# Optimization experiments

Hardware: AMD Instinct MI355X
Metric: run time of the kernel (lower is better)

The kernel has to match this reference:

```python
import jax, jax.numpy as jnp
import numpy as np
from jax import lax

W_SCALE = 0.1   # brevitas SignedBinaryWeightPerTensorConst default scaling_init
A_SCALE = 1.0   # SignedBinaryActPerTensorConst: min/max = -1/1 -> scale 1
BN_EPS = 1e-5


def _bin_w(w):
    # sign(w) * const scale, straight-through estimator (identity STE as in brevitas binary_sign_ste)
    q = jnp.where(w >= 0, W_SCALE, -W_SCALE).astype(w.dtype)
    return w + lax.stop_gradient(q - w)


def _bin_act(x):
    # QuantHardTanh with binary act quant: output is sign(x)*1, STE passes grad inside [-1,1]
    c = jnp.clip(x, -A_SCALE, A_SCALE)
    q = jnp.where(x >= 0, A_SCALE, -A_SCALE).astype(x.dtype)
    return c + lax.stop_gradient(q - c)


def _conv(x, w, b, stride=(1, 1), pad=((0, 0), (0, 0))):
    y = lax.conv_general_dilated(x, _bin_w(w), window_strides=stride, padding=pad,
                                 dimension_numbers=('NCHW', 'OIHW', 'NCHW'))
    return y + b[None, :, None, None]


def _bn(x, gamma, beta):
    # training-mode BatchNorm2d: batch statistics over (N, H, W)
    mu = jnp.mean(x, axis=(0, 2, 3), keepdims=True)
    var = jnp.var(x, axis=(0, 2, 3), keepdims=True)
    inv = lax.rsqrt(var + BN_EPS)
    return (x - mu) * inv * gamma[None, :, None, None] + beta[None, :, None, None]


def _pool2x1(x):
    # MaxPool2d((2,1)) with floor: drop trailing odd row
    N, C, H, W = x.shape
    h2 = H // 2
    return x[:, :, : 2 * h2].reshape(N, C, h2, 2, W).max(axis=3)


def setup_inputs() -> dict:
    key = jax.random.key(0)
    ks = jax.random.split(key, 10)
    nC = 128
    d = {
        'x':  jax.random.normal(ks[0], (64, 1, 16000, 1), jnp.float32),
        'w1': jax.random.normal(ks[1], (nC, 1, 84, 1), jnp.float32) * 0.05,
        'b1': jnp.zeros((nC,), jnp.float32),
        'g1': jnp.ones((nC,), jnp.float32), 'be1': jnp.zeros((nC,), jnp.float32),
        'w2': jax.random.normal(ks[2], (nC, nC, 4, 1), jnp.float32) * 0.05,
        'b2': jnp.zeros((nC,), jnp.float32),
        'g2': jnp.ones((nC,), jnp.float32), 'be2': jnp.zeros((nC,), jnp.float32),
        'w3': jax.random.normal(ks[3], (2 * nC, nC, 4, 1), jnp.float32) * 0.05,
        'b3': jnp.zeros((2 * nC,), jnp.float32),
        'g3': jnp.ones((2 * nC,), jnp.float32), 'be3': jnp.zeros((2 * nC,), jnp.float32),
        'w5': jax.random.normal(ks[4], (4 * nC, 2 * nC, 3, 1), jnp.float32) * 0.05,
        'b5': jnp.zeros((4 * nC,), jnp.float32),
        'g5': jnp.ones((4 * nC,), jnp.float32), 'be5': jnp.zeros((4 * nC,), jnp.float32),
        'wfc': jax.random.normal(ks[5], (35, 4 * nC * 249), jnp.float32) * 0.01,
    }
    return d


def reference(x, w1, b1, g1, be1, w2, b2, g2, be2, w3, b3, g3, be3,
              w5, b5, g5, be5, wfc):
    h = _conv(x, w1, b1, stride=(4, 1))                     # [B,128,3980,1]
    h = _pool2x1(_bin_act(_bn(h, g1, be1)))                 # [B,128,1990,1]
    h = _conv(h, w2, b2, pad=((2, 2), (0, 0)))              # [B,128,1991,1]
    h = _pool2x1(_bin_act(_bn(h, g2, be2)))                 # [B,128,995,1]
    h = _conv(h, w3, b3, pad=((1, 1), (0, 0)))              # [B,256,994,1]
    h = _pool2x1(_bin_act(_bn(h, g3, be3)))                 # [B,256,497,1]
    h = _conv(h, w5, b5, pad=((2, 2), (0, 0)))              # [B,512,499,1]
    h = _pool2x1(_bin_act(_bn(h, g5, be5)))                 # [B,512,249,1]
    h = h.reshape(h.shape[0], -1)                           # [B, 512*249]
    return h @ _bin_w(wfc).T                                # [B, 35]
```

## Files before the change

### kernel.cpp

```cpp
#include <hip/hip_runtime.h>
#include <stdint.h>


constexpr int Bn  = 64;
constexpr int H1  = 3980;
constexpr int J1  = 1990;
constexpr int H2o = 1991, J2 = 995;
constexpr int H3o = 994,  J3 = 497;
constexpr int H5o = 499,  J5 = 249;
constexpr int FCW = 249 * 8;
constexpr int NSH = 16;
constexpr int QS2 = 0;
constexpr int QS3 = 4096;
constexpr int QS5 = 12288;
constexpr int QS_TOTAL = 28672;

__global__ __launch_bounds__(256) void prep_all(
    const float* __restrict__ w2, const float* __restrict__ w3,
    const float* __restrict__ w5, const float* __restrict__ wfc,
    const float* __restrict__ w1,
    uint64_t* __restrict__ wb2, uint64_t* __restrict__ wb3,
    uint64_t* __restrict__ wb5, uint64_t* __restrict__ wbf,
    float* __restrict__ w1pk, unsigned long long* __restrict__ qs)
{
    const int bx  = blockIdx.x;
    const int idx = bx * 256 + threadIdx.x;
    if (idx < QS_TOTAL) qs[idx] = 0ull;

    if (bx < 78) {
        if (idx < 1024) {
            int wdx = idx & 1, k = (idx >> 1) & 3, c = idx >> 3;
            uint64_t v = 0;
            for (int ci = 0; ci < 64; ++ci)
                if (w2[((size_t)c * 128 + (wdx * 64 + ci)) * 4 + k] >= 0.f) v |= 1ull << ci;
            wb2[idx] = v;
        } else if (idx < 3072) {
            int t = idx - 1024;
            int wdx = t & 1, k = (t >> 1) & 3, c = t >> 3;
            uint64_t v = 0;
            for (int ci = 0; ci < 64; ++ci)
                if (w3[((size_t)c * 128 + (wdx * 64 + ci)) * 4 + k] >= 0.f) v |= 1ull << ci;
            wb3[t] = v;
        } else if (idx < 9216) {
            int t = idx - 3072;
            int wdx = t & 3, k = (t >> 2) % 3, c = t / 12;
            uint64_t v = 0;
            for (int ci = 0; ci < 64; ++ci)
                if (w5[((size_t)c * 256 + (wdx * 64 + ci)) * 3 + k] >= 0.f) v |= 1ull << ci;
            wb5[t] = v;
        } else if (idx < 9216 + 10752) {
            int t  = idx - 9216;
            int G  = t / 672, r = t % 672;
            int kg = r >> 5;
            int e  = r & 31;
            int u  = e >> 2, jj = e & 3;
            w1pk[t] = (w1[(size_t)(G * 8 + u) * 84 + kg * 4 + jj] >= 0.f) ? 0.1f : -0.1f;
        }
    } else {
        const int t = bx - 78;
        const int oc = t >> 3, wdx = t & 7;
        const int wave = threadIdx.x >> 6, lane = threadIdx.x & 63;
        const int hh = wave * 64 + lane;
        const bool ok = hh < 249;
        const float* src = wfc + (size_t)oc * 127488 + (size_t)wdx * 64 * 249 + hh;
        uint64_t word = 0;
        #pragma unroll 8
        for (int c = 0; c < 64; ++c) {
            const float v = ok ? src[(size_t)c * 249] : -1.f;
            if (v >= 0.f) word |= 1ull << c;
        }
        if (ok) wbf[(size_t)oc * FCW + (size_t)hh * 8 + wdx] = word;
    }
}

#define ROW_FMA(A, XV) \
    A[u] = fmaf(wv.x, XV.x, A[u]); A[u] = fmaf(wv.y, XV.y, A[u]); \
    A[u] = fmaf(wv.z, XV.z, A[u]); A[u] = fmaf(wv.w, XV.w, A[u]);
#define ROW_STAT(A, HOFF) { \
    const int h = h0 + (HOFF) + tid; \
    if (h < H1) { const float v = A[u] + bv; base[h] = v; \
                  s += (double)v; q += (double)v * v; } }

__global__ __launch_bounds__(256) void conv1_y1(
    const float* __restrict__ x, const float4* __restrict__ w1pk,
    const float* __restrict__ b1, float* __restrict__ y1,
    double2* __restrict__ part)
{
    __shared__ float4 xs4[2068];
    __shared__ float4 wl[336];
    __shared__ double2 statw[4][16];
    const int n   = blockIdx.y;
    const int bh  = blockIdx.x;
    const int h0  = bh << 11;
    const int z   = blockIdx.z;
    const int tid = threadIdx.x;
    const int wave = tid >> 6, lane = tid & 63;

    const float4* x4 = (const float4*)x + (size_t)n * 4000;
    for (int i = tid; i < 2068; i += 256) {
        const int gi = h0 + i;
        xs4[i] = (gi < 4000) ? x4[gi] : make_float4(0.f, 0.f, 0.f, 0.f);
    }
    const float4* wsrc = w1pk + (size_t)z * 336;
    for (int i = tid; i < 336; i += 256) wl[i] = wsrc[i];
    __syncthreads();

    for (int g = 0; g < 2; ++g) {
        float a0[8] = {0,0,0,0,0,0,0,0};
        float a1r[8] = {0,0,0,0,0,0,0,0};
        float a2[8] = {0,0,0,0,0,0,0,0};
        float a3[8] = {0,0,0,0,0,0,0,0};
        float a4[8] = {0,0,0,0,0,0,0,0};
        float a5[8] = {0,0,0,0,0,0,0,0};
        float a6[8] = {0,0,0,0,0,0,0,0};
        float a7[8] = {0,0,0,0,0,0,0,0};
        #pragma unroll 3
        for (int kg = 0; kg < 21; ++kg) {
            const float4 xv0 = xs4[tid + kg];
            const float4 xv1 = xs4[tid + 256 + kg];
            const float4 xv2 = xs4[tid + 512 + kg];
            const float4 xv3 = xs4[tid + 768 + kg];
            const float4 xv4 = xs4[tid + 1024 + kg];
            const float4 xv5 = xs4[tid + 1280 + kg];
            const float4 xv6 = xs4[tid + 1536 + kg];
            const float4 xv7 = xs4[tid + 1792 + kg];
            const float4* wk = &wl[(g * 21 + kg) * 8];
            #pragma unroll
            for (int u = 0; u < 8; ++u) {
                const float4 wv = wk[u];
                ROW_FMA(a0, xv0)
                ROW_FMA(a1r, xv1)
                ROW_FMA(a2, xv2)
                ROW_FMA(a3, xv3)
                ROW_FMA(a4, xv4)
                ROW_FMA(a5, xv5)
                ROW_FMA(a6, xv6)
                ROW_FMA(a7, xv7)
            }
        }
        #pragma unroll
        for (int u = 0; u < 8; ++u) {
            const int c = z * 16 + g * 8 + u;
            const float bv = b1[c];
            float* base = y1 + ((size_t)n * 128 + c) * H1;
            double s = 0.0, q = 0.0;
            ROW_STAT(a0, 0)
            ROW_STAT(a1r, 256)
            ROW_STAT(a2, 512)
            ROW_STAT(a3, 768)
            ROW_STAT(a4, 1024)
            ROW_STAT(a5, 1280)
            ROW_STAT(a6, 1536)
            ROW_STAT(a7, 1792)
            #pragma unroll
            for (int o = 32; o > 0; o >>= 1) {
                s += __shfl_xor(s, o, 64);
                q += __shfl_xor(q, o, 64);
            }
            if (lane == 0) statw[wave][g * 8 + u] = make_double2(s, q);
        }
    }
    __syncthreads();
    if (tid < 16) {
        const double2 p0 = statw[0][tid], p1v = statw[1][tid];
        const double2 p2 = statw[2][tid], p3  = statw[3][tid];
        part[((size_t)((n * 2 + bh) * 8 + z)) * 16 + tid] =
            make_double2(((p0.x + p1v.x) + p2.x) + p3.x,
                         ((p0.y + p1v.y) + p2.y) + p3.y);
    }
}

__global__ __launch_bounds__(128) void bn_reduce1(const double2* __restrict__ part,
                                                  float2* __restrict__ bnp)
{
    __shared__ double sS[128], sQ[128];
    const int c = blockIdx.x, t = threadIdx.x;
    const int z = c >> 4, cl = c & 15;
    const double2 p = part[((size_t)(t * 8 + z)) * 16 + cl];
    sS[t] = p.x; sQ[t] = p.y;
    __syncthreads();
    for (int o = 64; o > 0; o >>= 1) {
        if (t < o) { sS[t] += sS[t + o]; sQ[t] += sQ[t + o]; }
        __syncthreads();
    }
    if (t == 0) {
        const double N = (double)Bn * H1;
        const double mu  = sS[0] / N;
        const double var = sQ[0] / N - mu * mu;
        bnp[c] = make_float2((float)mu, (float)(1.0 / sqrt(var + 1e-5)));
    }
}

__global__ __launch_bounds__(256) void signpool1_y(
    const float* __restrict__ y1, const float2* __restrict__ bnp,
    const float* __restrict__ g1, const float* __restrict__ be1,
    uint32_t* __restrict__ a1_32)
{
    __shared__ float2 smi[128];
    __shared__ float  sg[128], sbe[128];
    const int n    = blockIdx.y;
    const int half = blockIdx.z;
    const int tid  = threadIdx.x;
    if (tid < 128) { smi[tid] = bnp[tid]; sg[tid] = g1[tid]; sbe[tid] = be1[tid]; }
    __syncthreads();
    const int j2  = blockIdx.x * 128 + (tid & 127);
    const int sub = tid >> 7;
    if (j2 >= 995) return;
    const int cbase = half * 64 + sub * 32;
    uint32_t wa = 0, wb = 0;
    for (int i = 0; i < 32; ++i) {
        const int c = cbase + i;
        const float4 v = *(const float4*)(y1 + ((size_t)n * 128 + c) * H1 + 4 * j2);
        const float2 mi = smi[c];
        const float gg = sg[c], bb = sbe[c];
        const float t0 = __fadd_rn(__fmul_rn(__fmul_rn(__fsub_rn(v.x, mi.x), mi.y), gg), bb);
        const float t1 = __fadd_rn(__fmul_rn(__fmul_rn(__fsub_rn(v.y, mi.x), mi.y), gg), bb);
        const float t2 = __fadd_rn(__fmul_rn(__fmul_rn(__fsub_rn(v.z, mi.x), mi.y), gg), bb);
        const float t3 = __fadd_rn(__fmul_rn(__fmul_rn(__fsub_rn(v.w, mi.x), mi.y), gg), bb);
        if ((t0 >= 0.f) || (t1 >= 0.f)) wa |= 1u << i;
        if ((t2 >= 0.f) || (t3 >= 0.f)) wb |= 1u << i;
    }
    const size_t w0 = ((size_t)n * J1 + 2 * j2) * 2 + half;
    a1_32[w0 * 2 + sub]       = wa;
    a1_32[(w0 + 2) * 2 + sub] = wb;
}

template<int CINW, int KK, int PAD, int COUT>
__global__ __launch_bounds__(COUT) void bconv_stats(
    const uint64_t* __restrict__ ain, const uint64_t* __restrict__ wb,
    const int HIN, const int HOUT, unsigned long long* __restrict__ qs)
{
    constexpr int RW = 64 + KK - 1;
    __shared__ ulonglong2 rows2[RW * CINW / 2];
    uint64_t* rows = (uint64_t*)rows2;
    const int n  = blockIdx.y;
    const int h0 = blockIdx.x << 6;
    const int c  = threadIdx.x;
    for (int i = c; i < RW * CINW; i += COUT) {
        int r = h0 - PAD + i / CINW;
        rows[i] = (r >= 0 && r < HIN) ? ain[((size_t)n * HIN + r) * CINW + (i % CINW)] : 0ull;
    }
    __syncthreads();
    uint64_t wreg[KK * CINW];
    #pragma unroll
    for (int i = 0; i < KK * CINW; ++i) wreg[i] = wb[(size_t)c * KK * CINW + i];
    int pcw[KK];
    #pragma unroll
    for (int k = 0; k < KK; ++k) {
        int pc = 0;
        #pragma unroll
        for (int wd = 0; wd < CINW; ++wd) pc += __popcll(wreg[k * CINW + wd]);
        pcw[k] = pc;
    }
    int sq = 0, sq2 = 0;
    const int hmax = min(64, HOUT - h0);
    int i = 0;
    for (; i + 1 < hmax; i += 2) {
        uint64_t win[(KK + 1) * CINW];
        #pragma unroll
        for (int t = 0; t < (KK + 1) * CINW / 2; ++t) {
            const ulonglong2 v = rows2[i * (CINW / 2) + t];
            win[2 * t] = v.x; win[2 * t + 1] = v.y;
        }
        int X0 = 0, X1 = 0;
        #pragma unroll
        for (int k = 0; k < KK; ++k)
            #pragma unroll
            for (int wd = 0; wd < CINW; ++wd) {
                X0 += __popcll(win[k * CINW + wd] ^ wreg[k * CINW + wd]);
                X1 += __popcll(win[(k + 1) * CINW + wd] ^ wreg[k * CINW + wd]);
            }
        int q0 = 64 * CINW * KK - 2 * X0;
        int q1 = 64 * CINW * KK - 2 * X1;
        const int h = h0 + i;
        if (h < PAD || h + 1 > HIN + PAD - KK) {
            #pragma unroll
            for (int k = 0; k < KK; ++k) {
                if (k < PAD - h || k >= HIN + PAD - h)
                    q0 -= 64 * CINW - 2 * pcw[k];
                if (k < PAD - (h + 1) || k >= HIN + PAD - (h + 1))
                    q1 -= 64 * CINW - 2 * pcw[k];
            }
        }
        sq += q0 + q1; sq2 += q0 * q0 + q1 * q1;
    }
    if (i < hmax) {
        const int h = h0 + i;
        int X = 0;
        #pragma unroll
        for (int k = 0; k < KK; ++k)
            #pragma unroll
            for (int wd = 0; wd < CINW; ++wd)
                X += __popcll(rows[(i + k) * CINW + wd] ^ wreg[k * CINW + wd]);
        int q = 64 * CINW * KK - 2 * X;
        if (h < PAD || h > HIN + PAD - KK) {
            #pragma unroll
            for (int k = 0; k < KK; ++k)
                if (k < PAD - h || k >= HIN + PAD - h)
                    q -= 64 * CINW - 2 * pcw[k];
        }
        sq += q; sq2 += q * q;
    }
    const int sh = (blockIdx.x + blockIdx.y) & (NSH - 1);
    atomicAdd(&qs[((size_t)sh * COUT + c) * 2 + 0], (unsigned long long)(long long)sq);
    atomicAdd(&qs[((size_t)sh * COUT + c) * 2 + 1], (unsigned long long)(long long)sq2);
}

template<int CINW, int KK, int PAD, int COUT>
__global__ __launch_bounds__(COUT) void bconv_sign(
    const uint64_t* __restrict__ ain, const uint64_t* __restrict__ wb,
    const int HIN, const int HOUT, const int J, const double N,
    const float* __restrict__ bias, const unsigned long long* __restrict__ qs,
    const float* __restrict__ g, const float* __restrict__ be,
    uint64_t* __restrict__ aout)
{
    constexpr int W = COUT / 64;
    constexpr int RW = 64 + KK - 1;
    __shared__ ulonglong2 rows2[RW * CINW / 2];
    uint64_t* rows = (uint64_t*)rows2;
    const int n  = blockIdx.y;
    const int h0 = blockIdx.x << 6;
    const int c  = threadIdx.x;
    for (int i = c; i < RW * CINW; i += COUT) {
        int r = h0 - PAD + i / CINW;
        rows[i] = (r >= 0 && r < HIN) ? ain[((size_t)n * HIN + r) * CINW + (i % CINW)] : 0ull;
    }
    long long Sq = 0, Sq2 = 0;
    #pragma unroll
    for (int s = 0; s < NSH; ++s) {
        Sq  += (long long)qs[((size_t)s * COUT + c) * 2 + 0];
        Sq2 += (long long)qs[((size_t)s * COUT + c) * 2 + 1];
    }
    const double bb_d = (double)bias[c];
    const double S  = 0.1 * (double)Sq + N * bb_d;
    const double SS = 0.01 * (double)Sq2 + 0.2 * bb_d * (double)Sq + N * bb_d * bb_d;
    const double mu = S / N;
    const double var = SS / N - mu * mu;
    const float2 mi = make_float2((float)mu, (float)(1.0 / sqrt(var + 1e-5)));
    __syncthreads();
    uint64_t wreg[KK * CINW];
    #pragma unroll
    for (int i = 0; i < KK * CINW; ++i) wreg[i] = wb[(size_t)c * KK * CINW + i];
    int pcw[KK];
    #pragma unroll
    for (int k = 0; k < KK; ++k) {
        int pc = 0;
        #pragma unroll
        for (int wd = 0; wd < CINW; ++wd) pc += __popcll(wreg[k * CINW + wd]);
        pcw[k] = pc;
    }
    const float bb = bias[c], gg = g[c], bbe = be[c];
    const int wv = c >> 6, lane = c & 63;
    const int hmax = min(64, HOUT - h0);
    for (int i = 0; i + 1 < hmax; i += 2) {
        uint64_t win[(KK + 1) * CINW];
        #pragma unroll
        for (int t = 0; t < (KK + 1) * CINW / 2; ++t) {
            const ulonglong2 v = rows2[i * (CINW / 2) + t];
            win[2 * t] = v.x; win[2 * t + 1] = v.y;
        }
        int X0 = 0, X1 = 0;
        #pragma unroll
        for (int k = 0; k < KK; ++k)
            #pragma unroll
            for (int wd = 0; wd < CINW; ++wd) {
                X0 += __popcll(win[k * CINW + wd] ^ wreg[k * CINW + wd]);
                X1 += __popcll(win[(k + 1) * CINW + wd] ^ wreg[k * CINW + wd]);
            }
        int q0 = 64 * CINW * KK - 2 * X0;
        int q1 = 64 * CINW * KK - 2 * X1;
        const int h = h0 + i;
        if (h < PAD || h + 1 > HIN + PAD - KK) {
            #pragma unroll
            for (int k = 0; k < KK; ++k) {
                if (k < PAD - h || k >= HIN + PAD - h)
                    q0 -= 64 * CINW - 2 * pcw[k];
                if (k < PAD - (h + 1) || k >= HIN + PAD - (h + 1))
                    q1 -= 64 * CINW - 2 * pcw[k];
            }
        }
        const float y0 = __fadd_rn(__fmul_rn(0.1f, (float)q0), bb);
        const float y1v = __fadd_rn(__fmul_rn(0.1f, (float)q1), bb);
        const float t0 = __fadd_rn(__fmul_rn(__fmul_rn(__fsub_rn(y0,  mi.x), mi.y), gg), bbe);
        const float t1 = __fadd_rn(__fmul_rn(__fmul_rn(__fsub_rn(y1v, mi.x), mi.y), gg), bbe);
        const uint64_t word = __ballot(t0 >= 0.f) | __ballot(t1 >= 0.f);
        const int j = h >> 1;
        if (lane == 0 && j < J)
            aout[((size_t)n * J + j) * W + wv] = word;
    }
}

__global__ void fc_kernel(const uint64_t* __restrict__ a5, const uint64_t* __restrict__ wfcb,
                          float* __restrict__ out)
{
    const int n    = blockIdx.y;
    const int oc   = blockIdx.x * 4 + (threadIdx.x >> 6);
    const int lane = threadIdx.x & 63;
    if (oc >= 35) return;
    const uint64_t* arow = a5   + (size_t)n  * FCW;
    const uint64_t* wrow = wfcb + (size_t)oc * FCW;
    int X = 0;
    for (int i = lane; i < FCW; i += 64)
        X += __popcll(arow[i] ^ wrow[i]);
    for (int o = 32; o > 0; o >>= 1) X += __shfl_xor(X, o, 64);
    if (lane == 0) out[(size_t)n * 35 + oc] = 0.1f * (float)(127488 - 2 * X);
}

extern "C" void kernel_launch(void* const* d_in, const int* in_sizes, int n_in,
                              void* d_out, int out_size, void* d_ws, size_t ws_size,
                              hipStream_t stream)
{
    (void)in_sizes; (void)n_in; (void)out_size;
    const float* x   = (const float*)d_in[0];
    const float* w1  = (const float*)d_in[1];
    const float* b1  = (const float*)d_in[2];
    const float* g1  = (const float*)d_in[3];
    const float* be1 = (const float*)d_in[4];
    const float* w2  = (const float*)d_in[5];
    const float* b2  = (const float*)d_in[6];
    const float* g2  = (const float*)d_in[7];
    const float* be2 = (const float*)d_in[8];
    const float* w3  = (const float*)d_in[9];
    const float* b3  = (const float*)d_in[10];
    const float* g3  = (const float*)d_in[11];
    const float* be3 = (const float*)d_in[12];
    const float* w5  = (const float*)d_in[13];
    const float* b5  = (const float*)d_in[14];
    const float* g5  = (const float*)d_in[15];
    const float* be5 = (const float*)d_in[16];
    const float* wfc = (const float*)d_in[17];
    char* ws = (char*)d_ws;

    size_t cur = 0;
    auto take = [&](size_t bytes) {
        size_t r = cur;
        cur = (cur + bytes + 255) & ~(size_t)255;
        return r;
    };
    const size_t off_y1 = take(130416640);
    float*    y1  = (float*)(ws + off_y1);
    uint64_t* a1  = (uint64_t*)(ws + take(2037760));
    uint64_t* a2  = (uint64_t*)(ws + take(1018880));
    uint64_t* a3  = (uint64_t*)(ws + take(1017856));
    uint64_t* a5  = (uint64_t*)(ws + take(1019904));
    uint64_t* wb2 = (uint64_t*)(ws + take(8192));
    uint64_t* wb3 = (uint64_t*)(ws + take(16384));
    uint64_t* wb5 = (uint64_t*)(ws + take(49152));
    uint64_t* wbf = (uint64_t*)(ws + take(557760));
    float*    w1pk = (float*)(ws + take(43008));
    double2*  p1  = (double2*)(ws + take(262144));
    unsigned long long* qs = (unsigned long long*)(ws + take(QS_TOTAL * 8));
    float2*   bnp1 = (float2*)(ws + take(1024));
    if (cur > ws_size) return;

    hipLaunchKernelGGL(prep_all, dim3(358), dim3(256), 0, stream,
                       w2, w3, w5, wfc, w1, wb2, wb3, wb5, wbf, w1pk, qs);
    hipLaunchKernelGGL(conv1_y1, dim3(2, 64, 8), dim3(256), 0, stream,
                       x, (const float4*)w1pk, b1, y1, p1);
    hipLaunchKernelGGL(bn_reduce1, dim3(128), dim3(128), 0, stream, p1, bnp1);
    hipLaunchKernelGGL(signpool1_y, dim3(8, 64, 2), dim3(256), 0, stream,
                       y1, bnp1, g1, be1, (uint32_t*)a1);
    hipLaunchKernelGGL((bconv_stats<2, 4, 2, 128>), dim3(32, 64), dim3(128), 0, stream,
                       a1, wb2, J1, H2o, qs + QS2);
    hipLaunchKernelGGL((bconv_sign<2, 4, 2, 128>), dim3(32, 64), dim3(128), 0, stream,
                       a1, wb2, J1, H2o, J2, (double)Bn * H2o, b2, qs + QS2, g2, be2, a2);
    hipLaunchKernelGGL((bconv_stats<2, 4, 1, 256>), dim3(16, 64), dim3(256), 0, stream,
                       a2, wb3, J2, H3o, qs + QS3);
    hipLaunchKernelGGL((bconv_sign<2, 4, 1, 256>), dim3(16, 64), dim3(256), 0, stream,
                       a2, wb3, J2, H3o, J3, (double)Bn * H3o, b3, qs + QS3, g3, be3, a3);
    hipLaunchKernelGGL((bconv_stats<4, 3, 2, 512>), dim3(8, 64), dim3(512), 0, stream,
                       a3, wb5, J3, H5o, qs + QS5);
    hipLaunchKernelGGL((bconv_sign<4, 3, 2, 512>), dim3(8, 64), dim3(512), 0, stream,
                       a3, wb5, J3, H5o, J5, (double)Bn * H5o, b5, qs + QS5, g5, be5, a5);
    hipLaunchKernelGGL(fc_kernel, dim3(9, 64), dim3(256), 0, stream,
                       a5, wbf, (float*)d_out);
}
```

Before: 304.2 us.

## Fuse post-conv1 stages into one cooperative persistent kernel with grid syncs

Replaces the chain of small kernels (BN reduce, sign-pool, three conv stats/sign pairs, FC) with a single cooperative kernel of 512 persistent blocks. Grid-wide syncs separate the phases, and blocks loop over virtual blocks. Conv phases now use fixed 256-thread blocks and split rows or channels to fit that size. The goal is to remove per-kernel launch and drain overhead between many short stages. The cost is the grid.sync barriers, fewer resident blocks per phase, and register pressure from one large kernel.

After: 726.9 us. +139.0%, slower.

```diff
diff --git a/kernel.cpp b/kernel.cpp
--- a/kernel.cpp
+++ b/kernel.cpp
@@ -1,5 +1,8 @@
 #include <hip/hip_runtime.h>
+#include <hip/hip_cooperative_groups.h>
 #include <stdint.h>
+
+namespace cg = cooperative_groups;
 
 
 constexpr int Bn  = 64;
@@ -14,6 +17,7 @@
 constexpr int QS3 = 4096;
 constexpr int QS5 = 12288;
 constexpr int QS_TOTAL = 28672;
+constexpr int MEGA_BLOCKS = 512;
 
 __global__ __launch_bounds__(256) void prep_all(
     const float* __restrict__ w2, const float* __restrict__ w3,
@@ -170,240 +174,244 @@
     }
 }
 
-__global__ __launch_bounds__(128) void bn_reduce1(const double2* __restrict__ part,
-                                                  float2* __restrict__ bnp)
+struct MegaArgs {
+    const double2* p1;
+    float2* bnp1;
+    const float* g1; const float* be1;
+    const float* y1;
+    uint32_t* a1_32;
+    const uint64_t* a1;
+    const uint64_t* wb2; const uint64_t* wb3; const uint64_t* wb5;
+    const uint64_t* wbf;
+    unsigned long long* qs;
+    const float* b2; const float* g2; const float* be2;
+    const float* b3; const float* g3; const float* be3;
+    const float* b5; const float* g5; const float* be5;
+    uint64_t* a2; uint64_t* a3; uint64_t* a5;
+    float* out;
+};
+
+template<int CINW, int KK, int PAD, int COUT, int NSUB, int CSPL, bool SIGN>
+__device__ void bconv_phase(const uint64_t* __restrict__ ain,
+                            const uint64_t* __restrict__ wbt,
+                            const int HIN, const int HOUT, const int J,
+                            const double N, const float* __restrict__ bias,
+                            unsigned long long* __restrict__ qs,
+                            const float* __restrict__ g, const float* __restrict__ be,
+                            uint64_t* __restrict__ aout, ulonglong2* rows2)
 {
+    constexpr int CPB = COUT / CSPL;
+    constexpr int TR  = 64 * NSUB;
+    constexpr int WR  = TR + KK - 1;
+    constexpr int W   = COUT / 64;
+    uint64_t* rows = (uint64_t*)rows2;
+    const int tid = threadIdx.x;
+    const int sub = tid / CPB;
+    const int cl  = tid % CPB;
+    const int ntiles = (HOUT + TR - 1) / TR;
+    const int nvb = ntiles * CSPL * 64;
+
+    for (int vb = blockIdx.x; vb < nvb; vb += gridDim.x) {
+        const int tile  = vb % ntiles;
+        const int rest  = vb / ntiles;
+        const int chunk = rest % CSPL;
+        const int n     = rest / CSPL;
+        const int c     = chunk * CPB + cl;
+        const int h0    = tile * TR;
+        __syncthreads();
+        for (int i = tid; i < WR * CINW; i += 256) {
+            const int r = h0 - PAD + i / CINW;
+            rows[i] = (r >= 0 && r < HIN) ? ain[((size_t)n * HIN + r) * CINW + (i % CINW)] : 0ull;
+        }
+        __syncthreads();
+        uint64_t wreg[KK * CINW];
+        #pragma unroll
+        for (int i2 = 0; i2 < KK * CINW; ++i2) wreg[i2] = wbt[(size_t)c * KK * CINW + i2];
+        int pcw[KK];
+        #pragma unroll
+        for (int k = 0; k < KK; ++k) {
+            int pc = 0;
+            #pragma unroll
+            for (int wd = 0; wd < CINW; ++wd) pc += __popcll(wreg[k * CINW + wd]);
+            pcw[k] = pc;
+        }
+        const int hb   = h0 + sub * 64;
+        const int hmax = min(64, HOUT - hb);
+        float2 mi = make_float2(0.f, 0.f);
+        float bb = 0.f, gg = 0.f, bbe = 0.f;
+        if constexpr (SIGN) {
+            long long Sq = 0, Sq2 = 0;
+            #pragma unroll
+            for (int s = 0; s < NSH; ++s) {
+                Sq  += (long long)qs[((size_t)s * COUT + c) * 2 + 0];
+                Sq2 += (long long)qs[((size_t)s * COUT + c) * 2 + 1];
+            }
+            const double bb_d = (double)bias[c];
+            const double S  = 0.1 * (double)Sq + N * bb_d;
+            const double SS = 0.01 * (double)Sq2 + 0.2 * bb_d * (double)Sq + N * bb_d * bb_d;
+            const double mu = S / N;
+            const double var = SS / N - mu * mu;
+            mi = make_float2((float)mu, (float)(1.0 / sqrt(var + 1e-5)));
+            bb = bias[c]; gg = g[c]; bbe = be[c];
+        }
+        int sq = 0, sq2 = 0;
+        int i = 0;
+        for (; i + 1 < hmax; i += 2) {
+            const int l = sub * 64 + i;
+            uint64_t win[(KK + 1) * CINW];
+            #pragma unroll
+            for (int t2 = 0; t2 < (KK + 1) * CINW / 2; ++t2) {
+                const ulonglong2 v = rows2[l * (CINW / 2) + t2];
+                win[2 * t2] = v.x; win[2 * t2 + 1] = v.y;
+            }
+            int X0 = 0, X1 = 0;
+            #pragma unroll
+            for (int k = 0; k < KK; ++k)
+                #pragma unroll
+                for (int wd = 0; wd < CINW; ++wd) {
+                    X0 += __popcll(win[k * CINW + wd] ^ wreg[k * CINW + wd]);
+                    X1 += __popcll(win[(k + 1) * CINW + wd] ^ wreg[k * CINW + wd]);
+                }
+            int q0 = 64 * CINW * KK - 2 * X0;
+            int q1 = 64 * CINW * KK - 2 * X1;
+            const int h = hb + i;
+            if (h < PAD || h + 1 > HIN + PAD - KK) {
+                #pragma unroll
+                for (int k = 0; k < KK; ++k) {
+                    if (k < PAD - h || k >= HIN + PAD - h)
+                        q0 -= 64 * CINW - 2 * pcw[k];
+                    if (k < PAD - (h + 1) || k >= HIN + PAD - (h + 1))
+                        q1 -= 64 * CINW - 2 * pcw[k];
+                }
+            }
+            if constexpr (SIGN) {
+                const float y0  = __fadd_rn(__fmul_rn(0.1f, (float)q0), bb);
+                const float y1v = __fadd_rn(__fmul_rn(0.1f, (float)q1), bb);
+                const float t0 = __fadd_rn(__fmul_rn(__fmul_rn(__fsub_rn(y0,  mi.x), mi.y), gg), bbe);
+                const float t1 = __fadd_rn(__fmul_rn(__fmul_rn(__fsub_rn(y1v, mi.x), mi.y), gg), bbe);
+                const uint64_t word = __ballot(t0 >= 0.f) | __ballot(t1 >= 0.f);
+                const int j = h >> 1;
+                if ((c & 63) == 0 && j < J)
+                    aout[((size_t)n * J + j) * W + (c >> 6)] = word;
+            } else {
+                sq += q0 + q1; sq2 += q0 * q0 + q1 * q1;
+            }
+        }
+        if constexpr (!SIGN) {
+            if (i < hmax) {
+                const int l = sub * 64 + i;
+                const int h = hb + i;
+                int X = 0;
+                #pragma unroll
+                for (int k = 0; k < KK; ++k)
+                    #pragma unroll
+                    for (int wd = 0; wd < CINW; ++wd)
+                        X += __popcll(rows[(l + k) * CINW + wd] ^ wreg[k * CINW + wd]);
+                int q = 64 * CINW * KK - 2 * X;
+                if (h < PAD || h > HIN + PAD - KK) {
+                    #pragma unroll
+                    for (int k = 0; k < KK; ++k)
+                        if (k < PAD - h || k >= HIN + PAD - h)
+                            q -= 64 * CINW - 2 * pcw[k];
+                }
+                sq += q; sq2 += q * q;
+            }
+            const int sh = vb & (NSH - 1);
+            atomicAdd(&qs[((size_t)sh * COUT + c) * 2 + 0], (unsigned long long)(long long)sq);
+            atomicAdd(&qs[((size_t)sh * COUT + c) * 2 + 1], (unsigned long long)(long long)sq2);
+        }
+    }
+}
+
+__global__ __launch_bounds__(256) void mega(MegaArgs A)
+{
+    cg::grid_group grid = cg::this_grid();
     __shared__ double sS[128], sQ[128];
-    const int c = blockIdx.x, t = threadIdx.x;
-    const int z = c >> 4, cl = c & 15;
-    const double2 p = part[((size_t)(t * 8 + z)) * 16 + cl];
-    sS[t] = p.x; sQ[t] = p.y;
+    __shared__ float2 smi[128];
+    __shared__ float  sgm[128], sbe[128];
+    __shared__ ulonglong2 rows2[132];
+    const int tid = threadIdx.x;
+
+    if (blockIdx.x < 128) {
+        const int c = blockIdx.x;
+        const int z = c >> 4, cl = c & 15;
+        if (tid < 128) {
+            const double2 p = A.p1[((size_t)(tid * 8 + z)) * 16 + cl];
+            sS[tid] = p.x; sQ[tid] = p.y;
+        }
+        __syncthreads();
+        for (int o = 64; o > 0; o >>= 1) {
+            if (tid < o) { sS[tid] += sS[tid + o]; sQ[tid] += sQ[tid + o]; }
+            __syncthreads();
+        }
+        if (tid == 0) {
+            const double N = (double)Bn * H1;
+            const double mu  = sS[0] / N;
+            const double var = sQ[0] / N - mu * mu;
+            A.bnp1[c] = make_float2((float)mu, (float)(1.0 / sqrt(var + 1e-5)));
+        }
+    }
+    grid.sync();
+
+    if (tid < 128) { smi[tid] = A.bnp1[tid]; sgm[tid] = A.g1[tid]; sbe[tid] = A.be1[tid]; }
     __syncthreads();
-    for (int o = 64; o > 0; o >>= 1) {
-        if (t < o) { sS[t] += sS[t + o]; sQ[t] += sQ[t + o]; }
-        __syncthreads();
-    }
-    if (t == 0) {
-        const double N = (double)Bn * H1;
-        const double mu  = sS[0] / N;
-        const double var = sQ[0] / N - mu * mu;
-        bnp[c] = make_float2((float)mu, (float)(1.0 / sqrt(var + 1e-5)));
-    }
-}
-
-__global__ __launch_bounds__(256) void signpool1_y(
-    const float* __restrict__ y1, const float2* __restrict__ bnp,
-    const float* __restrict__ g1, const float* __restrict__ be1,
-    uint32_t* __restrict__ a1_32)
-{
-    __shared__ float2 smi[128];
-    __shared__ float  sg[128], sbe[128];
-    const int n    = blockIdx.y;
-    const int half = blockIdx.z;
-    const int tid  = threadIdx.x;
-    if (tid < 128) { smi[tid] = bnp[tid]; sg[tid] = g1[tid]; sbe[tid] = be1[tid]; }
-    __syncthreads();
-    const int j2  = blockIdx.x * 128 + (tid & 127);
-    const int sub = tid >> 7;
-    if (j2 >= 995) return;
-    const int cbase = half * 64 + sub * 32;
-    uint32_t wa = 0, wb = 0;
-    for (int i = 0; i < 32; ++i) {
-        const int c = cbase + i;
-        const float4 v = *(const float4*)(y1 + ((size_t)n * 128 + c) * H1 + 4 * j2);
-        const float2 mi = smi[c];
-        const float gg = sg[c], bb = sbe[c];
-        const float t0 = __fadd_rn(__fmul_rn(__fmul_rn(__fsub_rn(v.x, mi.x), mi.y), gg), bb);
-        const float t1 = __fadd_rn(__fmul_rn(__fmul_rn(__fsub_rn(v.y, mi.x), mi.y), gg), bb);
-        const float t2 = __fadd_rn(__fmul_rn(__fmul_rn(__fsub_rn(v.z, mi.x), mi.y), gg), bb);
-        const float t3 = __fadd_rn(__fmul_rn(__fmul_rn(__fsub_rn(v.w, mi.x), mi.y), gg), bb);
-        if ((t0 >= 0.f) || (t1 >= 0.f)) wa |= 1u << i;
-        if ((t2 >= 0.f) || (t3 >= 0.f)) wb |= 1u << i;
-    }
-    const size_t w0 = ((size_t)n * J1 + 2 * j2) * 2 + half;
-    a1_32[w0 * 2 + sub]       = wa;
-    a1_32[(w0 + 2) * 2 + sub] = wb;
-}
-
-template<int CINW, int KK, int PAD, int COUT>
-__global__ __launch_bounds__(COUT) void bconv_stats(
-    const uint64_t* __restrict__ ain, const uint64_t* __restrict__ wb,
-    const int HIN, const int HOUT, unsigned long long* __restrict__ qs)
-{
-    constexpr int RW = 64 + KK - 1;
-    __shared__ ulonglong2 rows2[RW * CINW / 2];
-    uint64_t* rows = (uint64_t*)rows2;
-    const int n  = blockIdx.y;
-    const int h0 = blockIdx.x << 6;
-    const int c  = threadIdx.x;
-    for (int i = c; i < RW * CINW; i += COUT) {
-        int r = h0 - PAD + i / CINW;
-        rows[i] = (r >= 0 && r < HIN) ? ain[((size_t)n * HIN + r) * CINW + (i % CINW)] : 0ull;
-    }
-    __syncthreads();
-    uint64_t wreg[KK * CINW];
-    #pragma unroll
-    for (int i = 0; i < KK * CINW; ++i) wreg[i] = wb[(size_t)c * KK * CINW + i];
-    int pcw[KK];
-    #pragma unroll
-    for (int k = 0; k < KK; ++k) {
-        int pc = 0;
+    for (int vb = blockIdx.x; vb < 1024; vb += gridDim.x) {
+        const int bx = vb & 7, n = (vb >> 3) & 63, half = vb >> 9;
+        const int j2 = bx * 128 + (tid & 127);
+        const int sub = tid >> 7;
+        if (j2 < 995) {
+            const int cbase = half * 64 + sub * 32;
+            uint32_t wa = 0, wbv = 0;
+            for (int i = 0; i < 32; ++i) {
+                const int c = cbase + i;
+                const float4 v = *(const float4*)(A.y1 + ((size_t)n * 128 + c) * H1 + 4 * j2);
+                const float2 mi = smi[c];
+                const float gg = sgm[c], bb = sbe[c];
+                const float t0 = __fadd_rn(__fmul_rn(__fmul_rn(__fsub_rn(v.x, mi.x), mi.y), gg), bb);
+                const float t1 = __fadd_rn(__fmul_rn(__fmul_rn(__fsub_rn(v.y, mi.x), mi.y), gg), bb);
+                const float t2 = __fadd_rn(__fmul_rn(__fmul_rn(__fsub_rn(v.z, mi.x), mi.y), gg), bb);
+                const float t3 = __fadd_rn(__fmul_rn(__fmul_rn(__fsub_rn(v.w, mi.x), mi.y), gg), bb);
+                if ((t0 >= 0.f) || (t1 >= 0.f)) wa  |= 1u << i;
+                if ((t2 >= 0.f) || (t3 >= 0.f)) wbv |= 1u << i;
+            }
+            const size_t w0 = ((size_t)n * J1 + 2 * j2) * 2 + half;
+            A.a1_32[w0 * 2 + sub]       = wa;
+            A.a1_32[(w0 + 2) * 2 + sub] = wbv;
+        }
+    }
+    grid.sync();
+
+    bconv_phase<2, 4, 2, 128, 2, 1, false>(A.a1, A.wb2, J1, H2o, 0, 0.0, nullptr,
+                                           A.qs + QS2, nullptr, nullptr, nullptr, rows2);
+    grid.sync();
+    bconv_phase<2, 4, 2, 128, 2, 1, true>(A.a1, A.wb2, J1, H2o, J2, (double)Bn * H2o,
+                                          A.b2, A.qs + QS2, A.g2, A.be2, A.a2, rows2);
+    grid.sync();
+    bconv_phase<2, 4, 1, 256, 1, 1, false>(A.a2, A.wb3, J2, H3o, 0, 0.0, nullptr,
+                                           A.qs + QS3, nullptr, nullptr, nullptr, rows2);
+    grid.sync();
+    bconv_phase<2, 4, 1, 256, 1, 1, true>(A.a2, A.wb3, J2, H3o, J3, (double)Bn * H3o,
+                                          A.b3, A.qs + QS3, A.g3, A.be3, A.a3, rows2);
+    grid.sync();
+    bconv_phase<4, 3, 2, 512, 1, 2, false>(A.a3, A.wb5, J3, H5o, 0, 0.0, nullptr,
+                                           A.qs + QS5, nullptr, nullptr, nullptr, rows2);
+    grid.sync();
+    bconv_phase<4, 3, 2, 512, 1, 2, true>(A.a3, A.wb5, J3, H5o, J5, (double)Bn * H5o,
+                                          A.b5, A.qs + QS5, A.g5, A.be5, A.a5, rows2);
+    grid.sync();
+
+    for (int t = blockIdx.x * 4 + (tid >> 6); t < 64 * 35; t += gridDim.x * 4) {
+        const int n = t / 35, oc = t % 35;
+        const int lane = tid & 63;
+        const uint64_t* arow = A.a5  + (size_t)n  * FCW;
+        const uint64_t* wrow = A.wbf + (size_t)oc * FCW;
+        int X = 0;
+        for (int i = lane; i < FCW; i += 64)
+            X += __popcll(arow[i] ^ wrow[i]);
         #pragma unroll
-        for (int wd = 0; wd < CINW; ++wd) pc += __popcll(wreg[k * CINW + wd]);
-        pcw[k] = pc;
-    }
-    int sq = 0, sq2 = 0;
-    const int hmax = min(64, HOUT - h0);
-    int i = 0;
-    for (; i + 1 < hmax; i += 2) {
-        uint64_t win[(KK + 1) * CINW];
-        #pragma unroll
-        for (int t = 0; t < (KK + 1) * CINW / 2; ++t) {
-            const ulonglong2 v = rows2[i * (CINW / 2) + t];
-            win[2 * t] = v.x; win[2 * t + 1] = v.y;
-        }
-        int X0 = 0, X1 = 0;
-        #pragma unroll
-        for (int k = 0; k < KK; ++k)
-            #pragma unroll
-            for (int wd = 0; wd < CINW; ++wd) {
-                X0 += __popcll(win[k * CINW + wd] ^ wreg[k * CINW + wd]);
-                X1 += __popcll(win[(k + 1) * CINW + wd] ^ wreg[k * CINW + wd]);
-            }
-        int q0 = 64 * CINW * KK - 2 * X0;
-        int q1 = 64 * CINW * KK - 2 * X1;
-        const int h = h0 + i;
-        if (h < PAD || h + 1 > HIN + PAD - KK) {
-            #pragma unroll
-            for (int k = 0; k < KK; ++k) {
-                if (k < PAD - h || k >= HIN + PAD - h)
-                    q0 -= 64 * CINW - 2 * pcw[k];
-                if (k < PAD - (h + 1) || k >= HIN + PAD - (h + 1))
-                    q1 -= 64 * CINW - 2 * pcw[k];
-            }
-        }
-        sq += q0 + q1; sq2 += q0 * q0 + q1 * q1;
-    }
-    if (i < hmax) {
-        const int h = h0 + i;
-        int X = 0;
-        #pragma unroll
-        for (int k = 0; k < KK; ++k)
-            #pragma unroll
-            for (int wd = 0; wd < CINW; ++wd)
-                X += __popcll(rows[(i + k) * CINW + wd] ^ wreg[k * CINW + wd]);
-        int q = 64 * CINW * KK - 2 * X;
-        if (h < PAD || h > HIN + PAD - KK) {
-            #pragma unroll
-            for (int k = 0; k < KK; ++k)
-                if (k < PAD - h || k >= HIN + PAD - h)
-                    q -= 64 * CINW - 2 * pcw[k];
-        }
-        sq += q; sq2 += q * q;
-    }
-    const int sh = (blockIdx.x + blockIdx.y) & (NSH - 1);
-    atomicAdd(&qs[((size_t)sh * COUT + c) * 2 + 0], (unsigned long long)(long long)sq);
-    atomicAdd(&qs[((size_t)sh * COUT + c) * 2 + 1], (unsigned long long)(long long)sq2);
-}
-
-template<int CINW, int KK, int PAD, int COUT>
-__global__ __launch_bounds__(COUT) void bconv_sign(
-    const uint64_t* __restrict__ ain, const uint64_t* __restrict__ wb,
-    const int HIN, const int HOUT, const int J, const double N,
-    const float* __restrict__ bias, const unsigned long long* __restrict__ qs,
-    const float* __restrict__ g, const float* __restrict__ be,
-    uint64_t* __restrict__ aout)
-{
-    constexpr int W = COUT / 64;
-    constexpr int RW = 64 + KK - 1;
-    __shared__ ulonglong2 rows2[RW * CINW / 2];
-    uint64_t* rows = (uint64_t*)rows2;
-    const int n  = blockIdx.y;
-    const int h0 = blockIdx.x << 6;
-    const int c  = threadIdx.x;
-    for (int i = c; i < RW * CINW; i += COUT) {
-        int r = h0 - PAD + i / CINW;
-        rows[i] = (r >= 0 && r < HIN) ? ain[((size_t)n * HIN + r) * CINW + (i % CINW)] : 0ull;
-    }
-    long long Sq = 0, Sq2 = 0;
-    #pragma unroll
-    for (int s = 0; s < NSH; ++s) {
-        Sq  += (long long)qs[((size_t)s * COUT + c) * 2 + 0];
-        Sq2 += (long long)qs[((size_t)s * COUT + c) * 2 + 1];
-    }
-    const double bb_d = (double)bias[c];
-    const double S  = 0.1 * (double)Sq + N * bb_d;
-    const double SS = 0.01 * (double)Sq2 + 0.2 * bb_d * (double)Sq + N * bb_d * bb_d;
-    const double mu = S / N;
-    const double var = SS / N - mu * mu;
-    const float2 mi = make_float2((float)mu, (float)(1.0 / sqrt(var + 1e-5)));
-    __syncthreads();
-    uint64_t wreg[KK * CINW];
-    #pragma unroll
-    for (int i = 0; i < KK * CINW; ++i) wreg[i] = wb[(size_t)c * KK * CINW + i];
-    int pcw[KK];
-    #pragma unroll
-    for (int k = 0; k < KK; ++k) {
-        int pc = 0;
-        #pragma unroll
-        for (int wd = 0; wd < CINW; ++wd) pc += __popcll(wreg[k * CINW + wd]);
-        pcw[k] = pc;
-    }
-    const float bb = bias[c], gg = g[c], bbe = be[c];
-    const int wv = c >> 6, lane = c & 63;
-    const int hmax = min(64, HOUT - h0);
-    for (int i = 0; i + 1 < hmax; i += 2) {
-        uint64_t win[(KK + 1) * CINW];
-        #pragma unroll
-        for (int t = 0; t < (KK + 1) * CINW / 2; ++t) {
-            const ulonglong2 v = rows2[i * (CINW / 2) + t];
-            win[2 * t] = v.x; win[2 * t + 1] = v.y;
-        }
-        int X0 = 0, X1 = 0;
-        #pragma unroll
-        for (int k = 0; k < KK; ++k)
-            #pragma unroll
-            for (int wd = 0; wd < CINW; ++wd) {
-                X0 += __popcll(win[k * CINW + wd] ^ wreg[k * CINW + wd]);
-                X1 += __popcll(win[(k + 1) * CINW + wd] ^ wreg[k * CINW + wd]);
-            }
-        int q0 = 64 * CINW * KK - 2 * X0;
-        int q1 = 64 * CINW * KK - 2 * X1;
-        const int h = h0 + i;
-        if (h < PAD || h + 1 > HIN + PAD - KK) {
-            #pragma unroll
-            for (int k = 0; k < KK; ++k) {
-                if (k < PAD - h || k >= HIN + PAD - h)
-                    q0 -= 64 * CINW - 2 * pcw[k];
-                if (k < PAD - (h + 1) || k >= HIN + PAD - (h + 1))
-                    q1 -= 64 * CINW - 2 * pcw[k];
-            }
-        }
-        const float y0 = __fadd_rn(__fmul_rn(0.1f, (float)q0), bb);
-        const float y1v = __fadd_rn(__fmul_rn(0.1f, (float)q1), bb);
-        const float t0 = __fadd_rn(__fmul_rn(__fmul_rn(__fsub_rn(y0,  mi.x), mi.y), gg), bbe);
-        const float t1 = __fadd_rn(__fmul_rn(__fmul_rn(__fsub_rn(y1v, mi.x), mi.y), gg), bbe);
-        const uint64_t word = __ballot(t0 >= 0.f) | __ballot(t1 >= 0.f);
-        const int j = h >> 1;
-        if (lane == 0 && j < J)
-            aout[((size_t)n * J + j) * W + wv] = word;
-    }
-}
-
-__global__ void fc_kernel(const uint64_t* __restrict__ a5, const uint64_t* __restrict__ wfcb,
-                          float* __restrict__ out)
-{
-    const int n    = blockIdx.y;
-    const int oc   = blockIdx.x * 4 + (threadIdx.x >> 6);
-    const int lane = threadIdx.x & 63;
-    if (oc >= 35) return;
-    const uint64_t* arow = a5   + (size_t)n  * FCW;
-    const uint64_t* wrow = wfcb + (size_t)oc * FCW;
-    int X = 0;
-    for (int i = lane; i < FCW; i += 64)
-        X += __popcll(arow[i] ^ wrow[i]);
-    for (int o = 32; o > 0; o >>= 1) X += __shfl_xor(X, o, 64);
-    if (lane == 0) out[(size_t)n * 35 + oc] = 0.1f * (float)(127488 - 2 * X);
+        for (int o = 32; o > 0; o >>= 1) X += __shfl_xor(X, o, 64);
+        if (lane == 0) A.out[(size_t)n * 35 + oc] = 0.1f * (float)(127488 - 2 * X);
+    }
 }
 
 extern "C" void kernel_launch(void* const* d_in, const int* in_sizes, int n_in,
@@ -457,21 +465,18 @@
                        w2, w3, w5, wfc, w1, wb2, wb3, wb5, wbf, w1pk, qs);
     hipLaunchKernelGGL(conv1_y1, dim3(2, 64, 8), dim3(256), 0, stream,
                        x, (const float4*)w1pk, b1, y1, p1);
-    hipLaunchKernelGGL(bn_reduce1, dim3(128), dim3(128), 0, stream, p1, bnp1);
-    hipLaunchKernelGGL(signpool1_y, dim3(8, 64, 2), dim3(256), 0, stream,
-                       y1, bnp1, g1, be1, (uint32_t*)a1);
-    hipLaunchKernelGGL((bconv_stats<2, 4, 2, 128>), dim3(32, 64), dim3(128), 0, stream,
-                       a1, wb2, J1, H2o, qs + QS2);
-    hipLaunchKernelGGL((bconv_sign<2, 4, 2, 128>), dim3(32, 64), dim3(128), 0, stream,
-                       a1, wb2, J1, H2o, J2, (double)Bn * H2o, b2, qs + QS2, g2, be2, a2);
-    hipLaunchKernelGGL((bconv_stats<2, 4, 1, 256>), dim3(16, 64), dim3(256), 0, stream,
-                       a2, wb3, J2, H3o, qs + QS3);
-    hipLaunchKernelGGL((bconv_sign<2, 4, 1, 256>), dim3(16, 64), dim3(256), 0, stream,
-                       a2, wb3, J2, H3o, J3, (double)Bn * H3o, b3, qs + QS3, g3, be3, a3);
-    hipLaunchKernelGGL((bconv_stats<4, 3, 2, 512>), dim3(8, 64), dim3(512), 0, stream,
-                       a3, wb5, J3, H5o, qs + QS5);
-    hipLaunchKernelGGL((bconv_sign<4, 3, 2, 512>), dim3(8, 64), dim3(512), 0, stream,
-                       a3, wb5, J3, H5o, J5, (double)Bn * H5o, b5, qs + QS5, g5, be5, a5);
-    hipLaunchKernelGGL(fc_kernel, dim3(9, 64), dim3(256), 0, stream,
-                       a5, wbf, (float*)d_out);
+
+    MegaArgs margs;
+    margs.p1 = p1; margs.bnp1 = bnp1; margs.g1 = g1; margs.be1 = be1;
+    margs.y1 = y1; margs.a1_32 = (uint32_t*)a1; margs.a1 = a1;
+    margs.wb2 = wb2; margs.wb3 = wb3; margs.wb5 = wb5; margs.wbf = wbf;
+    margs.qs = qs;
+    margs.b2 = b2; margs.g2 = g2; margs.be2 = be2;
+    margs.b3 = b3; margs.g3 = g3; margs.be3 = be3;
+    margs.b5 = b5; margs.g5 = g5; margs.be5 = be5;
+    margs.a2 = a2; margs.a3 = a3; margs.a5 = a5;
+    margs.out = (float*)d_out;
+    void* kp[] = { &margs };
+    hipLaunchCooperativeKernel((const void*)mega, dim3(MEGA_BLOCKS), dim3(256),
+                               kp, 0, stream);
 }
```
